# Optimization experiments

Hardware: AMD Instinct MI355X
Metric: run time of the kernel (lower is better)

## Reference

```python
import jax, jax.numpy as jnp
import numpy as np

N, NE = 100000, 1600000
D_NODE, D_EDGE, HID, HEADS = 64, 32, 64, 4
D_HEAD = HID // HEADS


def _ln(x, g, b, eps=1e-5):
    m = jnp.mean(x, axis=-1, keepdims=True)
    v = jnp.mean((x - m) ** 2, axis=-1, keepdims=True)
    return (x - m) / jnp.sqrt(v + eps) * g + b


def _segment_softmax(logits, seg, num_segments):
    # logits: [E, H]; softmax over edges sharing the same destination node
    m = jax.ops.segment_max(logits, seg, num_segments=num_segments)
    m = jnp.where(jnp.isfinite(m), m, 0.0)
    ex = jnp.exp(logits - m[seg])
    s = jax.ops.segment_sum(ex, seg, num_segments=num_segments)
    return ex / (s[seg] + 1e-16)


def _gtconv(x, edge_attr,
            WQ_w, WK_w, WV_w, WO_w, WO_b, WE_w, WE_b, WOe_w, WOe_b,
            ng_w, ng_b, eg_w, eg_b,
            ffn_w1, ffn_b1, ffn_w2, ffn_b2,
            ffne_w1, ffne_b1, ffne_w2, ffne_b2,
            n1_g, n1_b, n2_g, n2_b, n1e_g, n1e_b, n2e_g, n2e_b,
            edge_index):
    n = x.shape[0]
    src, dst = edge_index[0], edge_index[1]
    # QKV + node gate projections (qkv_bias=False)
    Q = (x @ WQ_w.T).reshape(n, HEADS, D_HEAD)
    K = (x @ WK_w.T).reshape(n, HEADS, D_HEAD)
    V = (x @ WV_w.T).reshape(n, HEADS, D_HEAD)
    G = (x @ ng_w.T + ng_b).reshape(n, HEADS, D_HEAD)
    # per-edge attention with edge-feature fusion
    Ef = (edge_attr @ WE_w.T + WE_b).reshape(-1, HEADS, D_HEAD)      # [E,H,d]
    qijk = Q[dst] * K[src] * Ef / jnp.sqrt(jnp.float32(D_HEAD))      # [E,H,d]
    eij = qijk                                                       # saved edge message
    logits = qijk.sum(axis=-1)                                       # [E,H]
    alpha = _segment_softmax(logits, dst, n)                         # [E,H]
    # gated values
    Eg = (edge_attr @ eg_w.T + eg_b).reshape(-1, HEADS, D_HEAD)
    gate = jax.nn.sigmoid(G[src] + Eg)                               # [E,H,d]
    msg = alpha[..., None] * gate * V[src]                           # [E,H,d]
    agg = jax.ops.segment_sum(msg.reshape(-1, HID), dst, num_segments=n)  # [N,HID]
    # node update (dropout=0 -> identity)
    out = agg @ WO_w.T + WO_b + x
    out = _ln(out, n1_g, n1_b)
    ffn = jax.nn.relu(out @ ffn_w1.T + ffn_b1) @ ffn_w2.T + ffn_b2
    out = _ln(out + ffn, n2_g, n2_b)
    # edge update
    e = eij.reshape(-1, HID)
    e = e @ WOe_w.T + WOe_b + edge_attr
    e = _ln(e, n1e_g, n1e_b)
    ffe = jax.nn.relu(e @ ffne_w1.T + ffne_b1) @ ffne_w2.T + ffne_b2
    e = _ln(e + ffe, n2e_g, n2e_b)
    return out, e


def setup_inputs() -> dict:
    key = jax.random.key(0)
    ks = jax.random.split(key, 24)
    f32 = jnp.float32

    def w(k, o, i):
        return (jax.random.normal(k, (o, i), dtype=f32) / np.sqrt(i)).astype(f32)

    inp = {
        "x": jax.random.normal(ks[0], (N, D_NODE), dtype=f32),
        "edge_attr": jax.random.normal(ks[1], (NE, D_EDGE), dtype=f32),
        "WQ_w": w(ks[2], HID, D_NODE), "WK_w": w(ks[3], HID, D_NODE), "WV_w": w(ks[4], HID, D_NODE),
        "WO_w": w(ks[5], D_NODE, HID), "WO_b": jnp.zeros((D_NODE,), f32),
        "WE_w": w(ks[6], HID, D_EDGE), "WE_b": jnp.zeros((HID,), f32),
        "WOe_w": w(ks[7], D_EDGE, HID), "WOe_b": jnp.zeros((D_EDGE,), f32),
        "ng_w": w(ks[8], HID, D_NODE), "ng_b": jnp.zeros((HID,), f32),
        "eg_w": w(ks[9], HID, D_EDGE), "eg_b": jnp.zeros((HID,), f32),
        "ffn_w1": w(ks[10], HID, D_NODE), "ffn_b1": jnp.zeros((HID,), f32),
        "ffn_w2": w(ks[11], D_NODE, HID), "ffn_b2": jnp.zeros((D_NODE,), f32),
        "ffne_w1": w(ks[12], HID, D_EDGE), "ffne_b1": jnp.zeros((HID,), f32),
        "ffne_w2": w(ks[13], D_EDGE, HID), "ffne_b2": jnp.zeros((D_EDGE,), f32),
        "n1_g": jnp.ones((D_NODE,), f32), "n1_b": jnp.zeros((D_NODE,), f32),
        "n2_g": jnp.ones((D_NODE,), f32), "n2_b": jnp.zeros((D_NODE,), f32),
        "n1e_g": jnp.ones((D_EDGE,), f32), "n1e_b": jnp.zeros((D_EDGE,), f32),
        "n2e_g": jnp.ones((D_EDGE,), f32), "n2e_b": jnp.zeros((D_EDGE,), f32),
        "edge_index": jax.random.randint(ks[14], (2, NE), 0, N, dtype=jnp.int32),
    }
    return inp


def reference(x, edge_attr, WQ_w, WK_w, WV_w, WO_w, WO_b, WE_w, WE_b, WOe_w, WOe_b,
              ng_w, ng_b, eg_w, eg_b, ffn_w1, ffn_b1, ffn_w2, ffn_b2,
              ffne_w1, ffne_b1, ffne_w2, ffne_b2,
              n1_g, n1_b, n2_g, n2_b, n1e_g, n1e_b, n2e_g, n2e_b, edge_index):
    return _gtconv(x, edge_attr, WQ_w, WK_w, WV_w, WO_w, WO_b, WE_w, WE_b, WOe_w, WOe_b,
                   ng_w, ng_b, eg_w, eg_b, ffn_w1, ffn_b1, ffn_w2, ffn_b2,
                   ffne_w1, ffne_b1, ffne_w2, ffne_b2,
                   n1_g, n1_b, n2_g, n2_b, n1e_g, n1e_b, n2e_g, n2e_b, edge_index)
```

## Files before the change

kernel.cpp:

```cpp
#include <hip/hip_runtime.h>
#include <math.h>

#define N_NODES 100000
#define N_EDGES 1600000

__global__ __launch_bounds__(256) void k_node_proj(
    const float* __restrict__ x,
    const float* __restrict__ WQ, const float* __restrict__ WK,
    const float* __restrict__ WV, const float* __restrict__ NG,
    const float* __restrict__ NGb,
    float* __restrict__ Qout, float* __restrict__ SRCout)
{
    int n = blockIdx.x * 256 + threadIdx.x;
    if (n >= N_NODES) return;

    float xr[64];
    const float4* xp = reinterpret_cast<const float4*>(x + (size_t)n * 64);
#pragma unroll
    for (int i = 0; i < 16; ++i) {
        float4 v = xp[i];
        xr[4*i+0] = v.x; xr[4*i+1] = v.y; xr[4*i+2] = v.z; xr[4*i+3] = v.w;
    }

    float4* qo = reinterpret_cast<float4*>(Qout + (size_t)n * 64);
    float4* so = reinterpret_cast<float4*>(SRCout + (size_t)n * 192);

    for (int o4 = 0; o4 < 16; ++o4) {
        float q[4] = {0.f,0.f,0.f,0.f};
        float k[4] = {0.f,0.f,0.f,0.f};
        float v[4] = {0.f,0.f,0.f,0.f};
        float g[4];
#pragma unroll
        for (int s = 0; s < 4; ++s) g[s] = NGb[o4*4+s];
#pragma unroll
        for (int j = 0; j < 64; ++j) {
            float xj = xr[j];
#pragma unroll
            for (int s = 0; s < 4; ++s) {
                int row = o4*4 + s;
                q[s] = fmaf(WQ[row*64+j], xj, q[s]);
                k[s] = fmaf(WK[row*64+j], xj, k[s]);
                v[s] = fmaf(WV[row*64+j], xj, v[s]);
                g[s] = fmaf(NG[row*64+j], xj, g[s]);
            }
        }
        qo[o4]      = make_float4(q[0], q[1], q[2], q[3]);
        so[o4]      = make_float4(k[0], k[1], k[2], k[3]);
        so[16+o4]   = make_float4(v[0], v[1], v[2], v[3]);
        so[32+o4]   = make_float4(g[0], g[1], g[2], g[3]);
    }
}

__global__ void k_transpose3(const float* __restrict__ A,
                             const float* __restrict__ B,
                             const float* __restrict__ C,
                             float* __restrict__ T)
{
    int m = blockIdx.x;
    const float* W = (m == 0) ? A : ((m == 1) ? B : C);
    float* O = T + (size_t)m * 4096;
    for (int k = threadIdx.x; k < 4096; k += 256) {
        int j = k >> 6, o = k & 63;
        O[k] = W[o*64 + j];
    }
}

__global__ __launch_bounds__(256) void k_edge(
    const float* __restrict__ ea_g,
    const int*   __restrict__ ei,
    const float* __restrict__ Q,   const float* __restrict__ SRC,
    const float* __restrict__ WE,  const float* __restrict__ WEb,
    const float* __restrict__ EG,  const float* __restrict__ EGb,
    const float* __restrict__ WOe, const float* __restrict__ WOeb,
    const float* __restrict__ W1,  const float* __restrict__ W1b,
    const float* __restrict__ W2,  const float* __restrict__ W2b,
    const float* __restrict__ g1,  const float* __restrict__ b1,
    const float* __restrict__ g2,  const float* __restrict__ b2,
    float* __restrict__ sden, float* __restrict__ agg,
    float* __restrict__ eout)
{
    int e = blockIdx.x * 256 + threadIdx.x;
    int src = ei[e];
    int dst = ei[N_EDGES + e];

    float ea[32];
    {
        const float4* eap = reinterpret_cast<const float4*>(ea_g + (size_t)e * 32);
#pragma unroll
        for (int i = 0; i < 8; ++i) {
            float4 t = eap[i];
            ea[4*i+0] = t.x; ea[4*i+1] = t.y; ea[4*i+2] = t.z; ea[4*i+3] = t.w;
        }
    }

    float emid[32];
#pragma unroll
    for (int j = 0; j < 32; ++j) emid[j] = 0.f;

    const float4* Qbase = reinterpret_cast<const float4*>(Q + (size_t)dst * 64);
    const float4* Sbase = reinterpret_cast<const float4*>(SRC + (size_t)src * 192);

    for (int h = 0; h < 4; ++h) {
        float Qd[16], Ks[16];
#pragma unroll
        for (int i = 0; i < 4; ++i) {
            float4 a = Qbase[h*4 + i];
            Qd[4*i+0]=a.x; Qd[4*i+1]=a.y; Qd[4*i+2]=a.z; Qd[4*i+3]=a.w;
            float4 b = Sbase[h*4 + i];
            Ks[4*i+0]=b.x; Ks[4*i+1]=b.y; Ks[4*i+2]=b.z; Ks[4*i+3]=b.w;
        }

        float qk[16];
        float logit = 0.f;
#pragma unroll
        for (int o = 0; o < 16; ++o) {
            float ef = WEb[h*16 + o];
#pragma unroll
            for (int j = 0; j < 32; ++j)
                ef = fmaf(WE[(h*16+o)*32 + j], ea[j], ef);
            float t = Qd[o] * Ks[o] * ef * 0.25f;
            qk[o] = t;
            logit += t;
        }

        float ex = __expf(logit);
        atomicAdd(&sden[(size_t)dst*4 + h], ex);

#pragma unroll
        for (int o = 0; o < 16; ++o) {
            float t = qk[o];
#pragma unroll
            for (int j = 0; j < 32; ++j)
                emid[j] = fmaf(WOe[j*64 + h*16 + o], t, emid[j]);
        }

        float Vs[16], Gs[16];
#pragma unroll
        for (int i = 0; i < 4; ++i) {
            float4 a = Sbase[16 + h*4 + i];
            Vs[4*i+0]=a.x; Vs[4*i+1]=a.y; Vs[4*i+2]=a.z; Vs[4*i+3]=a.w;
            float4 b = Sbase[32 + h*4 + i];
            Gs[4*i+0]=b.x; Gs[4*i+1]=b.y; Gs[4*i+2]=b.z; Gs[4*i+3]=b.w;
        }
#pragma unroll
        for (int o = 0; o < 16; ++o) {
            float eg = EGb[h*16 + o];
#pragma unroll
            for (int j = 0; j < 32; ++j)
                eg = fmaf(EG[(h*16+o)*32 + j], ea[j], eg);
            float gate = 1.f / (1.f + __expf(-(Gs[o] + eg)));
            atomicAdd(&agg[(size_t)dst*64 + h*16 + o], ex * gate * Vs[o]);
        }
    }

    float y[32];
    {
        float mean = 0.f;
#pragma unroll
        for (int j = 0; j < 32; ++j) {
            float t = emid[j] + WOeb[j] + ea[j];
            y[j] = t;
            mean += t;
        }
        mean *= (1.f/32.f);
        float var = 0.f;
#pragma unroll
        for (int j = 0; j < 32; ++j) { float d = y[j]-mean; var = fmaf(d,d,var); }
        var *= (1.f/32.f);
        float rs = rsqrtf(var + 1e-5f);
#pragma unroll
        for (int j = 0; j < 32; ++j)
            y[j] = (y[j]-mean)*rs*g1[j] + b1[j];
    }

    float ff[32];
#pragma unroll
    for (int j = 0; j < 32; ++j) ff[j] = W2b[j];
    for (int k = 0; k < 64; ++k) {
        float hk = W1b[k];
#pragma unroll
        for (int j = 0; j < 32; ++j)
            hk = fmaf(W1[k*32 + j], y[j], hk);
        hk = fmaxf(hk, 0.f);
#pragma unroll
        for (int j = 0; j < 32; ++j)
            ff[j] = fmaf(W2[j*64 + k], hk, ff[j]);
    }

    {
        float mean = 0.f;
#pragma unroll
        for (int j = 0; j < 32; ++j) { ff[j] += y[j]; mean += ff[j]; }
        mean *= (1.f/32.f);
        float var = 0.f;
#pragma unroll
        for (int j = 0; j < 32; ++j) { float d = ff[j]-mean; var = fmaf(d,d,var); }
        var *= (1.f/32.f);
        float rs = rsqrtf(var + 1e-5f);
#pragma unroll
        for (int j = 0; j < 32; ++j)
            ff[j] = (ff[j]-mean)*rs*g2[j] + b2[j];
    }

    float4* op = reinterpret_cast<float4*>(eout + (size_t)e * 32);
#pragma unroll
    for (int i = 0; i < 8; ++i)
        op[i] = make_float4(ff[4*i+0], ff[4*i+1], ff[4*i+2], ff[4*i+3]);
}

__global__ __launch_bounds__(256) void k_node_final(
    const float* __restrict__ agg, const float* __restrict__ sden,
    const float* __restrict__ x,
    const float* __restrict__ WOT, const float* __restrict__ WOb,
    const float* __restrict__ W1T, const float* __restrict__ W1b,
    const float* __restrict__ W2T, const float* __restrict__ W2b,
    const float* __restrict__ g1,  const float* __restrict__ b1,
    const float* __restrict__ g2,  const float* __restrict__ b2,
    float* __restrict__ outp)
{
    int gid  = blockIdx.x * 256 + threadIdx.x;
    int n    = gid >> 6;
    int lane = threadIdx.x & 63;
    if (n >= N_NODES) return;

    float a = agg[(size_t)n*64 + lane] / (sden[(size_t)n*4 + (lane>>4)] + 1e-16f);

    float acc = WOb[lane] + x[(size_t)n*64 + lane];
    for (int j = 0; j < 64; ++j)
        acc = fmaf(WOT[j*64 + lane], __shfl(a, j), acc);

    float s = acc;
    for (int off = 32; off; off >>= 1) s += __shfl_xor(s, off);
    float mean = s * (1.f/64.f);
    float d = acc - mean;
    float vs = d*d;
    for (int off = 32; off; off >>= 1) vs += __shfl_xor(vs, off);
    float rs = rsqrtf(vs*(1.f/64.f) + 1e-5f);
    float yv = d*rs*g1[lane] + b1[lane];

    float hk = W1b[lane];
    for (int j = 0; j < 64; ++j)
        hk = fmaf(W1T[j*64 + lane], __shfl(yv, j), hk);
    hk = fmaxf(hk, 0.f);
    float fo = W2b[lane];
    for (int k = 0; k < 64; ++k)
        fo = fmaf(W2T[k*64 + lane], __shfl(hk, k), fo);

    float u = yv + fo;
    float s2 = u;
    for (int off = 32; off; off >>= 1) s2 += __shfl_xor(s2, off);
    float mean2 = s2 * (1.f/64.f);
    float d2 = u - mean2;
    float v2 = d2*d2;
    for (int off = 32; off; off >>= 1) v2 += __shfl_xor(v2, off);
    float rs2 = rsqrtf(v2*(1.f/64.f) + 1e-5f);

    outp[(size_t)n*64 + lane] = d2*rs2*g2[lane] + b2[lane];
}

extern "C" void kernel_launch(void* const* d_in, const int* in_sizes, int n_in,
                              void* d_out, int out_size, void* d_ws, size_t ws_size,
                              hipStream_t stream)
{
    const float* x    = (const float*)d_in[0];
    const float* ea   = (const float*)d_in[1];
    const float* WQ   = (const float*)d_in[2];
    const float* WK   = (const float*)d_in[3];
    const float* WV   = (const float*)d_in[4];
    const float* WO   = (const float*)d_in[5];
    const float* WOb  = (const float*)d_in[6];
    const float* WE   = (const float*)d_in[7];
    const float* WEb  = (const float*)d_in[8];
    const float* WOe  = (const float*)d_in[9];
    const float* WOeb = (const float*)d_in[10];
    const float* NG   = (const float*)d_in[11];
    const float* NGb  = (const float*)d_in[12];
    const float* EGw  = (const float*)d_in[13];
    const float* EGb  = (const float*)d_in[14];
    const float* F1   = (const float*)d_in[15];
    const float* F1b  = (const float*)d_in[16];
    const float* F2   = (const float*)d_in[17];
    const float* F2b  = (const float*)d_in[18];
    const float* FE1  = (const float*)d_in[19];
    const float* FE1b = (const float*)d_in[20];
    const float* FE2  = (const float*)d_in[21];
    const float* FE2b = (const float*)d_in[22];
    const float* n1g  = (const float*)d_in[23];
    const float* n1b  = (const float*)d_in[24];
    const float* n2g  = (const float*)d_in[25];
    const float* n2b  = (const float*)d_in[26];
    const float* n1eg = (const float*)d_in[27];
    const float* n1eb = (const float*)d_in[28];
    const float* n2eg = (const float*)d_in[29];
    const float* n2eb = (const float*)d_in[30];
    const int*   ei   = (const int*)d_in[31];

    float* ws   = (float*)d_ws;
    float* sden = ws;
    float* agg  = ws + (size_t)N_NODES * 4;
    float* Q    = agg + (size_t)N_NODES * 64;
    float* SRC  = Q + (size_t)N_NODES * 64;
    float* TW   = SRC + (size_t)N_NODES * 192;

    float* out_nodes = (float*)d_out;
    float* out_edges = out_nodes + (size_t)N_NODES * 64;

    hipMemsetAsync(sden, 0, (size_t)N_NODES * 68 * sizeof(float), stream);

    k_transpose3<<<3, 256, 0, stream>>>(WO, F1, F2, TW);

    k_node_proj<<<(N_NODES + 255) / 256, 256, 0, stream>>>(
        x, WQ, WK, WV, NG, NGb, Q, SRC);

    k_edge<<<N_EDGES / 256, 256, 0, stream>>>(
        ea, ei, Q, SRC,
        WE, WEb, EGw, EGb, WOe, WOeb,
        FE1, FE1b, FE2, FE2b,
        n1eg, n1eb, n2eg, n2eb,
        sden, agg, out_edges);

    k_node_final<<<(N_NODES * 64 + 255) / 256, 256, 0, stream>>>(
        agg, sden, x,
        TW, WOb, TW + 4096, F1b, TW + 8192, F2b,
        n1g, n1b, n2g, n2b,
        out_nodes);
}
```

Before: 6.492 ms.

## Process one edge per wavefront with lane-parallel projections and shared-memory weights

Restructures the edge kernel from one thread per edge to one 64-lane wavefront per edge. Each lane owns one head-dim output, and dot products are formed by broadcasting edge features with readlane. Edge-update weights are staged transposed in LDS, and reductions use cross-lane shuffles. A persistent grid-stride loop over 1024 blocks replaces the old launch. This removes the huge per-thread register arrays and the uncoalesced per-thread gathers, and turns per-edge memory access into contiguous wave-wide loads. The cost is serialized 32/64-step readlane loops per edge, per-block weight staging, and many shuffles.

New measurement: 10.49 ms. 1.62x slower.

```diff
diff --git a/kernel.cpp b/kernel.cpp
--- a/kernel.cpp
+++ b/kernel.cpp
@@ -3,6 +3,10 @@
 
 #define N_NODES 100000
 #define N_EDGES 1600000
+
+__device__ __forceinline__ float bcast(float v, int srclane) {
+    return __uint_as_float(__builtin_amdgcn_readlane(__float_as_uint(v), srclane));
+}
 
 __global__ __launch_bounds__(256) void k_node_proj(
     const float* __restrict__ x,
@@ -65,7 +69,7 @@
     }
 }
 
-__global__ __launch_bounds__(256) void k_edge(
+__global__ __launch_bounds__(256, 4) void k_edge_fused(
     const float* __restrict__ ea_g,
     const int*   __restrict__ ei,
     const float* __restrict__ Q,   const float* __restrict__ SRC,
@@ -79,133 +83,130 @@
     float* __restrict__ sden, float* __restrict__ agg,
     float* __restrict__ eout)
 {
-    int e = blockIdx.x * 256 + threadIdx.x;
-    int src = ei[e];
-    int dst = ei[N_EDGES + e];
-
-    float ea[32];
+    __shared__ float sWOT[64*32];
+    __shared__ float sW1T[32*64];
+    __shared__ float sW2T[64*32];
+
+    const int tid  = threadIdx.x;
+    const int wid  = tid >> 6;
+    const int lane = tid & 63;
+    const int j32  = lane & 31;
+
+    for (int i = tid; i < 2048; i += 256) {
+        int k = i >> 5, j = i & 31;
+        sWOT[i] = WOe[j*64 + k];
+        sW2T[i] = W2[j*64 + k];
+    }
+    for (int i = tid; i < 2048; i += 256) {
+        int j = i >> 6, k = i & 63;
+        sW1T[i] = W1[k*32 + j];
+    }
+    __syncthreads();
+
+    float wet[32], egt[32];
     {
-        const float4* eap = reinterpret_cast<const float4*>(ea_g + (size_t)e * 32);
+        const float4* wp = reinterpret_cast<const float4*>(WE + (size_t)lane * 32);
+        const float4* gp = reinterpret_cast<const float4*>(EG + (size_t)lane * 32);
 #pragma unroll
         for (int i = 0; i < 8; ++i) {
-            float4 t = eap[i];
-            ea[4*i+0] = t.x; ea[4*i+1] = t.y; ea[4*i+2] = t.z; ea[4*i+3] = t.w;
-        }
-    }
-
-    float emid[32];
-#pragma unroll
-    for (int j = 0; j < 32; ++j) emid[j] = 0.f;
-
-    const float4* Qbase = reinterpret_cast<const float4*>(Q + (size_t)dst * 64);
-    const float4* Sbase = reinterpret_cast<const float4*>(SRC + (size_t)src * 192);
-
-    for (int h = 0; h < 4; ++h) {
-        float Qd[16], Ks[16];
-#pragma unroll
-        for (int i = 0; i < 4; ++i) {
-            float4 a = Qbase[h*4 + i];
-            Qd[4*i+0]=a.x; Qd[4*i+1]=a.y; Qd[4*i+2]=a.z; Qd[4*i+3]=a.w;
-            float4 b = Sbase[h*4 + i];
-            Ks[4*i+0]=b.x; Ks[4*i+1]=b.y; Ks[4*i+2]=b.z; Ks[4*i+3]=b.w;
-        }
-
-        float qk[16];
-        float logit = 0.f;
-#pragma unroll
-        for (int o = 0; o < 16; ++o) {
-            float ef = WEb[h*16 + o];
-#pragma unroll
-            for (int j = 0; j < 32; ++j)
-                ef = fmaf(WE[(h*16+o)*32 + j], ea[j], ef);
-            float t = Qd[o] * Ks[o] * ef * 0.25f;
-            qk[o] = t;
-            logit += t;
-        }
-
-        float ex = __expf(logit);
-        atomicAdd(&sden[(size_t)dst*4 + h], ex);
-
-#pragma unroll
-        for (int o = 0; o < 16; ++o) {
-            float t = qk[o];
-#pragma unroll
-            for (int j = 0; j < 32; ++j)
-                emid[j] = fmaf(WOe[j*64 + h*16 + o], t, emid[j]);
-        }
-
-        float Vs[16], Gs[16];
-#pragma unroll
-        for (int i = 0; i < 4; ++i) {
-            float4 a = Sbase[16 + h*4 + i];
-            Vs[4*i+0]=a.x; Vs[4*i+1]=a.y; Vs[4*i+2]=a.z; Vs[4*i+3]=a.w;
-            float4 b = Sbase[32 + h*4 + i];
-            Gs[4*i+0]=b.x; Gs[4*i+1]=b.y; Gs[4*i+2]=b.z; Gs[4*i+3]=b.w;
-        }
-#pragma unroll
-        for (int o = 0; o < 16; ++o) {
-            float eg = EGb[h*16 + o];
-#pragma unroll
-            for (int j = 0; j < 32; ++j)
-                eg = fmaf(EG[(h*16+o)*32 + j], ea[j], eg);
-            float gate = 1.f / (1.f + __expf(-(Gs[o] + eg)));
-            atomicAdd(&agg[(size_t)dst*64 + h*16 + o], ex * gate * Vs[o]);
-        }
-    }
-
-    float y[32];
-    {
-        float mean = 0.f;
+            float4 a = wp[i];
+            wet[4*i+0]=a.x; wet[4*i+1]=a.y; wet[4*i+2]=a.z; wet[4*i+3]=a.w;
+            float4 b = gp[i];
+            egt[4*i+0]=b.x; egt[4*i+1]=b.y; egt[4*i+2]=b.z; egt[4*i+3]=b.w;
+        }
+    }
+    const float wEb_r  = WEb[lane];
+    const float eGb_r  = EGb[lane];
+    const float w1b_r  = W1b[lane];
+    const float wOeb_r = WOeb[j32];
+    const float w2b_r  = W2b[j32];
+    const float g1_r   = g1[j32];
+    const float b1_r   = b1[j32];
+    const float g2_r   = g2[j32];
+    const float b2_r   = b2[j32];
+
+    const int stride = gridDim.x * 4;
+    for (int e = blockIdx.x * 4 + wid; e < N_EDGES; e += stride) {
+        const int eu  = __builtin_amdgcn_readfirstlane(e);
+        const int src = ei[eu];
+        const int dst = ei[N_EDGES + eu];
+
+        const float eav = ea_g[(size_t)eu*32 + j32];
+        const float qd  = Q[(size_t)dst*64 + lane];
+        const float ks  = SRC[(size_t)src*192 + lane];
+        const float vsv = SRC[(size_t)src*192 + 64 + lane];
+        const float gsv = SRC[(size_t)src*192 + 128 + lane];
+
+        float ef = wEb_r, eg = eGb_r;
 #pragma unroll
         for (int j = 0; j < 32; ++j) {
-            float t = emid[j] + WOeb[j] + ea[j];
-            y[j] = t;
-            mean += t;
-        }
-        mean *= (1.f/32.f);
-        float var = 0.f;
-#pragma unroll
-        for (int j = 0; j < 32; ++j) { float d = y[j]-mean; var = fmaf(d,d,var); }
-        var *= (1.f/32.f);
-        float rs = rsqrtf(var + 1e-5f);
+            float b = bcast(eav, j);
+            ef = fmaf(wet[j], b, ef);
+            eg = fmaf(egt[j], b, eg);
+        }
+
+        const float t = qd * ks * ef * 0.25f;
+
+        float lg = t;
+        lg += __shfl_xor(lg, 1);
+        lg += __shfl_xor(lg, 2);
+        lg += __shfl_xor(lg, 4);
+        lg += __shfl_xor(lg, 8);
+        const float ex = __expf(lg);
+
+        if ((lane & 15) == 0)
+            atomicAdd(&sden[(size_t)dst*4 + (lane >> 4)], ex);
+
+        const float gate = 1.f / (1.f + __expf(-(gsv + eg)));
+        atomicAdd(&agg[(size_t)dst*64 + lane], ex * gate * vsv);
+
+        float emid = 0.f;
+#pragma unroll
+        for (int k = 0; k < 64; ++k)
+            emid = fmaf(sWOT[k*32 + j32], bcast(t, k), emid);
+
+        float y = emid + wOeb_r + eav;
+        {
+            float s = y;
+            s += __shfl_xor(s, 1); s += __shfl_xor(s, 2);
+            s += __shfl_xor(s, 4); s += __shfl_xor(s, 8); s += __shfl_xor(s, 16);
+            float mean = s * (1.f/32.f);
+            float d = y - mean;
+            float v = d*d;
+            v += __shfl_xor(v, 1); v += __shfl_xor(v, 2);
+            v += __shfl_xor(v, 4); v += __shfl_xor(v, 8); v += __shfl_xor(v, 16);
+            float rs = rsqrtf(v*(1.f/32.f) + 1e-5f);
+            y = d*rs*g1_r + b1_r;
+        }
+
+        float h = w1b_r;
 #pragma unroll
         for (int j = 0; j < 32; ++j)
-            y[j] = (y[j]-mean)*rs*g1[j] + b1[j];
-    }
-
-    float ff[32];
-#pragma unroll
-    for (int j = 0; j < 32; ++j) ff[j] = W2b[j];
-    for (int k = 0; k < 64; ++k) {
-        float hk = W1b[k];
-#pragma unroll
-        for (int j = 0; j < 32; ++j)
-            hk = fmaf(W1[k*32 + j], y[j], hk);
-        hk = fmaxf(hk, 0.f);
-#pragma unroll
-        for (int j = 0; j < 32; ++j)
-            ff[j] = fmaf(W2[j*64 + k], hk, ff[j]);
-    }
-
-    {
-        float mean = 0.f;
-#pragma unroll
-        for (int j = 0; j < 32; ++j) { ff[j] += y[j]; mean += ff[j]; }
-        mean *= (1.f/32.f);
-        float var = 0.f;
-#pragma unroll
-        for (int j = 0; j < 32; ++j) { float d = ff[j]-mean; var = fmaf(d,d,var); }
-        var *= (1.f/32.f);
-        float rs = rsqrtf(var + 1e-5f);
-#pragma unroll
-        for (int j = 0; j < 32; ++j)
-            ff[j] = (ff[j]-mean)*rs*g2[j] + b2[j];
-    }
-
-    float4* op = reinterpret_cast<float4*>(eout + (size_t)e * 32);
-#pragma unroll
-    for (int i = 0; i < 8; ++i)
-        op[i] = make_float4(ff[4*i+0], ff[4*i+1], ff[4*i+2], ff[4*i+3]);
+            h = fmaf(sW1T[j*64 + lane], bcast(y, j), h);
+        h = fmaxf(h, 0.f);
+
+        float f2 = 0.f;
+#pragma unroll
+        for (int k = 0; k < 64; ++k)
+            f2 = fmaf(sW2T[k*32 + j32], bcast(h, k), f2);
+        f2 += w2b_r + y;
+
+        {
+            float s = f2;
+            s += __shfl_xor(s, 1); s += __shfl_xor(s, 2);
+            s += __shfl_xor(s, 4); s += __shfl_xor(s, 8); s += __shfl_xor(s, 16);
+            float mean = s * (1.f/32.f);
+            float d = f2 - mean;
+            float v = d*d;
+            v += __shfl_xor(v, 1); v += __shfl_xor(v, 2);
+            v += __shfl_xor(v, 4); v += __shfl_xor(v, 8); v += __shfl_xor(v, 16);
+            float rs = rsqrtf(v*(1.f/32.f) + 1e-5f);
+            f2 = d*rs*g2_r + b2_r;
+        }
+
+        if (lane < 32)
+            eout[(size_t)eu*32 + lane] = f2;
+    }
 }
 
 __global__ __launch_bounds__(256) void k_node_final(
@@ -312,7 +313,7 @@
     k_node_proj<<<(N_NODES + 255) / 256, 256, 0, stream>>>(
         x, WQ, WK, WV, NG, NGb, Q, SRC);
 
-    k_edge<<<N_EDGES / 256, 256, 0, stream>>>(
+    k_edge_fused<<<1024, 256, 0, stream>>>(
         ea, ei, Q, SRC,
         WE, WEb, EGw, EGb, WOe, WOeb,
         FE1, FE1b, FE2, FE2b,
```
